# Optimization experiments

Measured on AMD Instinct MI355X. Metric: run time of the kernel, lower is better.

The kernel has to match this reference:

```python
import jax, jax.numpy as jnp
import numpy as np

B, S, H = 1, 2048, 3584
NH, NKV, D = 16, 8, 256
GROUPS = NH // NKV
WINDOW = 1024
SOFTCAP = 50.0
SCALING = 256.0 ** -0.5  # query_pre_attn_scalar ** -0.5
MASK_VAL = -1e9


def rotate_half(x):
    x1, x2 = jnp.split(x, 2, axis=-1)
    return jnp.concatenate([-x2, x1], axis=-1)


def setup_inputs() -> dict:
    key = jax.random.key(0)
    ks = jax.random.split(key, 5)
    hidden_states = jax.random.normal(ks[0], (B, S, H), dtype=jnp.float32)
    # real rotary embeddings, HF convention: [B, S, head_dim]
    inv_freq = 1.0 / (10000.0 ** (np.arange(0, D, 2, dtype=np.float32) / D))
    freqs = np.arange(S, dtype=np.float32)[:, None] * inv_freq[None, :]  # [S, D/2]
    emb = np.concatenate([freqs, freqs], axis=-1)  # [S, D]
    cos = jnp.asarray(np.cos(emb))[None]  # [1, S, D]
    sin = jnp.asarray(np.sin(emb))[None]
    sc = 1.0 / np.sqrt(H)
    wq = jax.random.normal(ks[1], (NH * D, H), dtype=jnp.float32) * sc
    wk = jax.random.normal(ks[2], (NKV * D, H), dtype=jnp.float32) * sc
    wv = jax.random.normal(ks[3], (NKV * D, H), dtype=jnp.float32) * sc
    wo = jax.random.normal(ks[4], (H, NH * D), dtype=jnp.float32) * (1.0 / np.sqrt(NH * D))
    return {"hidden_states": hidden_states, "cos": cos, "sin": sin,
            "wq": wq, "wk": wk, "wv": wv, "wo": wo}


def reference(hidden_states, cos, sin, wq, wk, wv, wo):
    # QKV projections -> [B, n_heads, S, D]
    q = jnp.einsum('bsh,oh->bso', hidden_states, wq).reshape(B, S, NH, D).transpose(0, 2, 1, 3)
    k = jnp.einsum('bsh,oh->bso', hidden_states, wk).reshape(B, S, NKV, D).transpose(0, 2, 1, 3)
    v = jnp.einsum('bsh,oh->bso', hidden_states, wv).reshape(B, S, NKV, D).transpose(0, 2, 1, 3)
    # RoPE (cos/sin broadcast over head dim)
    c = cos[:, None, :, :]
    s = sin[:, None, :, :]
    q = q * c + rotate_half(q) * s
    k = k * c + rotate_half(k) * s
    # GQA: repeat KV heads
    k = jnp.repeat(k, GROUPS, axis=1)  # [B, NH, S, D]
    v = jnp.repeat(v, GROUPS, axis=1)
    # scores + logit soft-capping (tanh), then causal + sliding-window mask
    scores = jnp.einsum('bhqd,bhkd->bhqk', q, k) * SCALING
    scores = SOFTCAP * jnp.tanh(scores / SOFTCAP)
    idx = jnp.arange(S)
    allowed = (idx[None, :] <= idx[:, None]) & (idx[:, None] - idx[None, :] < WINDOW)  # [S, S]
    scores = jnp.where(allowed[None, None], scores, MASK_VAL)
    p = jax.nn.softmax(scores, axis=-1)
    out = jnp.einsum('bhqk,bhkd->bhqd', p, v)  # [B, NH, S, D]
    out = out.transpose(0, 2, 1, 3).reshape(B, S, NH * D)
    return jnp.einsum('bso,ho->bsh', out, wo)
```

## Files before the change

### kernel.cpp

```cpp
#include <hip/hip_runtime.h>
#include <stdint.h>

#define S_LEN 2048
#define HDIM  3584
#define NHEAD 16
#define NKVH  8
#define DHEAD 256
#define QD    (NHEAD * DHEAD)
#define KD    (NKVH * DHEAD)
#define QKVD  (QD + 2 * KD)
#define WINDOW 1024
#define MASK_VAL (-1e9f)

typedef __bf16 bf16x8 __attribute__((ext_vector_type(8)));
typedef float  f32x4  __attribute__((ext_vector_type(4)));

__device__ __forceinline__ float bf2f(ushort u) {
    union { uint32_t i; float f; } v; v.i = ((uint32_t)u) << 16; return v.f;
}
__device__ __forceinline__ ushort f2bf(float f) {
    union { float f; uint32_t i; } v; v.f = f;
    uint32_t r = (v.i + 0x7FFF + ((v.i >> 16) & 1)) >> 16;
    return (ushort)r;
}
__device__ __forceinline__ void gll16(const ushort* g, ushort* l) {
    __builtin_amdgcn_global_load_lds(
        (const __attribute__((address_space(1))) void*)g,
        (__attribute__((address_space(3))) void*)l, 16, 0, 0);
}

__global__ __launch_bounds__(256) void cvt_kernel(const float* __restrict__ src,
                                                  ushort* __restrict__ dst, int n8)
{
    int i = blockIdx.x * blockDim.x + threadIdx.x;
    if (i >= n8) return;
    float4 a = ((const float4*)src)[i * 2];
    float4 b = ((const float4*)src)[i * 2 + 1];
    ushort tmp[8];
    tmp[0] = f2bf(a.x); tmp[1] = f2bf(a.y); tmp[2] = f2bf(a.z); tmp[3] = f2bf(a.w);
    tmp[4] = f2bf(b.x); tmp[5] = f2bf(b.y); tmp[6] = f2bf(b.z); tmp[7] = f2bf(b.w);
    ((uint4*)dst)[i] = *(uint4*)tmp;
}

__device__ __forceinline__ void stage_f32(ushort* __restrict__ dst,
                                          const float* __restrict__ src,
                                          int r0, int K, int kt, int t)
{
#pragma unroll
    for (int i = 0; i < 4; i++) {
        int g = t + i * 256;
        int row = g >> 3, c = g & 7;
        float4 f = *(const float4*)(src + (size_t)(r0 + row) * K + kt + c * 4);
        ushort4 u;
        u.x = f2bf(f.x); u.y = f2bf(f.y); u.z = f2bf(f.z); u.w = f2bf(f.w);
        *(ushort4*)(dst + row * 32 + c * 4) = u;
    }
}

template <typename TA, typename TC>
__global__ __launch_bounds__(256) void gemm_async(const TA* __restrict__ A,
                                                  const ushort* __restrict__ B,
                                                  TC* __restrict__ C,
                                                  int M, int N, int K)
{
    __shared__ __align__(16) ushort As[128 * 32];
    __shared__ __align__(16) ushort Bs[128 * 32];

    const int t    = threadIdx.x;
    const int lane = t & 63;
    const int w    = t >> 6;
    const int l15  = lane & 15;
    const int quad = lane >> 4;
    const int m0   = blockIdx.y * 128;
    const int n0   = blockIdx.x * 128;
    const int wm   = (w >> 1) * 64;
    const int wn   = (w & 1) * 64;
    const int srow = lane >> 2;
    const int scol = (lane & 3) * 8;

    f32x4 acc[4][4] = {};

    for (int kt = 0; kt < K; kt += 32) {
        __syncthreads();
#pragma unroll
        for (int j = 0; j < 2; j++) {
            const int rb = w * 32 + j * 16;
            if constexpr (sizeof(TA) == 2) {
                gll16((const ushort*)A + (size_t)(m0 + rb + srow) * K + kt + scol,
                      As + rb * 32);
            }
            gll16(B + (size_t)(n0 + rb + srow) * K + kt + scol, Bs + rb * 32);
        }
        if constexpr (sizeof(TA) == 4)
            stage_f32(As, (const float*)A, m0, K, kt, t);
        __syncthreads();

        bf16x8 a[4], b[4];
#pragma unroll
        for (int mi = 0; mi < 4; mi++)
            a[mi] = *(const bf16x8*)(As + (wm + mi * 16 + l15) * 32 + quad * 8);
#pragma unroll
        for (int ni = 0; ni < 4; ni++)
            b[ni] = *(const bf16x8*)(Bs + (wn + ni * 16 + l15) * 32 + quad * 8);
#pragma unroll
        for (int mi = 0; mi < 4; mi++)
#pragma unroll
            for (int ni = 0; ni < 4; ni++)
                acc[mi][ni] = __builtin_amdgcn_mfma_f32_16x16x32_bf16(
                    a[mi], b[ni], acc[mi][ni], 0, 0, 0);
    }

#pragma unroll
    for (int mi = 0; mi < 4; mi++)
#pragma unroll
        for (int ni = 0; ni < 4; ni++)
#pragma unroll
            for (int r = 0; r < 4; r++) {
                int row = m0 + wm + mi * 16 + quad * 4 + r;
                int col = n0 + wn + ni * 16 + l15;
                float val = acc[mi][ni][r];
                if constexpr (sizeof(TC) == 4) C[(size_t)row * N + col] = val;
                else                           C[(size_t)row * N + col] = f2bf(val);
            }
}

__global__ __launch_bounds__(256) void gemm_sync(const float* __restrict__ A,
                                                 const float* __restrict__ B,
                                                 ushort* __restrict__ C,
                                                 int M, int N, int K)
{
    __shared__ __align__(16) ushort As[128 * 32];
    __shared__ __align__(16) ushort Bs[128 * 32];
    const int t = threadIdx.x, lane = t & 63, w = t >> 6;
    const int l15 = lane & 15, quad = lane >> 4;
    const int m0 = blockIdx.y * 128, n0 = blockIdx.x * 128;
    const int wm = (w >> 1) * 64, wn = (w & 1) * 64;
    f32x4 acc[4][4] = {};
    for (int kt = 0; kt < K; kt += 32) {
        __syncthreads();
        stage_f32(As, A, m0, K, kt, t);
        stage_f32(Bs, B, n0, K, kt, t);
        __syncthreads();
        bf16x8 a[4], b[4];
#pragma unroll
        for (int mi = 0; mi < 4; mi++)
            a[mi] = *(const bf16x8*)(As + (wm + mi * 16 + l15) * 32 + quad * 8);
#pragma unroll
        for (int ni = 0; ni < 4; ni++)
            b[ni] = *(const bf16x8*)(Bs + (wn + ni * 16 + l15) * 32 + quad * 8);
#pragma unroll
        for (int mi = 0; mi < 4; mi++)
#pragma unroll
            for (int ni = 0; ni < 4; ni++)
                acc[mi][ni] = __builtin_amdgcn_mfma_f32_16x16x32_bf16(
                    a[mi], b[ni], acc[mi][ni], 0, 0, 0);
    }
#pragma unroll
    for (int mi = 0; mi < 4; mi++)
#pragma unroll
        for (int ni = 0; ni < 4; ni++)
#pragma unroll
            for (int r = 0; r < 4; r++)
                C[(size_t)(m0 + wm + mi * 16 + quad * 4 + r) * N +
                  n0 + wn + ni * 16 + l15] = f2bf(acc[mi][ni][r]);
}

__global__ __launch_bounds__(256) void gemm_sync_hf(const ushort* __restrict__ A,
                                                    const float* __restrict__ B,
                                                    float* __restrict__ C,
                                                    int M, int N, int K)
{
    __shared__ __align__(16) ushort As[128 * 32];
    __shared__ __align__(16) ushort Bs[128 * 32];
    const int t = threadIdx.x, lane = t & 63, w = t >> 6;
    const int l15 = lane & 15, quad = lane >> 4;
    const int m0 = blockIdx.y * 128, n0 = blockIdx.x * 128;
    const int wm = (w >> 1) * 64, wn = (w & 1) * 64;
    f32x4 acc[4][4] = {};
    for (int kt = 0; kt < K; kt += 32) {
        __syncthreads();
#pragma unroll
        for (int i = 0; i < 2; i++) {
            int g = t + i * 256;
            int row = g >> 2, c = g & 3;
            *(uint4*)(As + row * 32 + c * 8) =
                *(const uint4*)(A + (size_t)(m0 + row) * K + kt + c * 8);
        }
        stage_f32(Bs, B, n0, K, kt, t);
        __syncthreads();
        bf16x8 a[4], b[4];
#pragma unroll
        for (int mi = 0; mi < 4; mi++)
            a[mi] = *(const bf16x8*)(As + (wm + mi * 16 + l15) * 32 + quad * 8);
#pragma unroll
        for (int ni = 0; ni < 4; ni++)
            b[ni] = *(const bf16x8*)(Bs + (wn + ni * 16 + l15) * 32 + quad * 8);
#pragma unroll
        for (int mi = 0; mi < 4; mi++)
#pragma unroll
            for (int ni = 0; ni < 4; ni++)
                acc[mi][ni] = __builtin_amdgcn_mfma_f32_16x16x32_bf16(
                    a[mi], b[ni], acc[mi][ni], 0, 0, 0);
    }
#pragma unroll
    for (int mi = 0; mi < 4; mi++)
#pragma unroll
        for (int ni = 0; ni < 4; ni++)
#pragma unroll
            for (int r = 0; r < 4; r++)
                C[(size_t)(m0 + wm + mi * 16 + quad * 4 + r) * N +
                  n0 + wn + ni * 16 + l15] = acc[mi][ni][r];
}

__global__ void rope_kernel(ushort* __restrict__ x, int stride,
                            const float* __restrict__ cosb,
                            const float* __restrict__ sinb, int nh)
{
    int idx  = blockIdx.x * blockDim.x + threadIdx.x;
    int d    = idx & 127;
    int rest = idx >> 7;
    int h    = rest & (nh - 1);
    int s    = rest / nh;
    size_t base = (size_t)s * stride + h * DHEAD;
    float c  = cosb[s * DHEAD + d];
    float sn = sinb[s * DHEAD + d];
    float x1 = bf2f(x[base + d]);
    float x2 = bf2f(x[base + d + 128]);
    x[base + d]       = f2bf(x1 * c - x2 * sn);
    x[base + d + 128] = f2bf(x2 * c + x1 * sn);
}

__global__ __launch_bounds__(256) void vtrans_kernel(const ushort* __restrict__ v,
                                                     int stride,
                                                     ushort* __restrict__ vt)
{
    __shared__ __align__(16) ushort tile[64][72];
    int s0 = blockIdx.x * 64, c0 = blockIdx.y * 64;
    int t  = threadIdx.x;
#pragma unroll
    for (int i = 0; i < 2; i++) {
        int cI = t + i * 256;
        int row = cI >> 3, c8 = cI & 7;
        *(uint4*)&tile[row][c8 * 8] =
            *(const uint4*)(v + (size_t)(s0 + row) * stride + c0 + c8 * 8);
    }
    __syncthreads();
#pragma unroll
    for (int i = 0; i < 2; i++) {
        int cI = t + i * 256;
        int crow = cI >> 3, s8 = cI & 7;
        ushort tmp[8];
#pragma unroll
        for (int j = 0; j < 8; j++) tmp[j] = tile[s8 * 8 + j][crow];
        *(uint4*)(vt + (size_t)(c0 + crow) * S_LEN + s0 + s8 * 8) = *(uint4*)tmp;
    }
}

template <typename TO>
__global__ __launch_bounds__(256) void attn_kernel(const ushort* __restrict__ qr, int qstride,
                                                   const ushort* __restrict__ kr, int kstride,
                                                   const ushort* __restrict__ vt,
                                                   TO* __restrict__ out)
{
    __shared__ __align__(16) ushort Ks[64 * 256];
    __shared__ __align__(16) ushort Vs[256 * 64];
    __shared__ __align__(16) ushort Ps[4][16 * 68];

    const int t    = threadIdx.x;
    const int lane = t & 63;
    const int w    = t >> 6;
    const int l15  = lane & 15;
    const int quad = lane >> 4;
    const int q0B  = blockIdx.x * 64;
    const int q0   = q0B + w * 16;
    const int h    = blockIdx.y;
    const int kvh  = h >> 1;

    bf16x8 aQ[8];
    const ushort* qrow = qr + (size_t)(q0 + l15) * qstride + h * DHEAD;
#pragma unroll
    for (int kk = 0; kk < 8; kk++)
        aQ[kk] = *(const bf16x8*)(qrow + kk * 32 + quad * 8);

    f32x4 oacc[16] = {};
    float m_i[4], l_i[4];
#pragma unroll
    for (int r = 0; r < 4; r++) { m_i[r] = -1e30f; l_i[r] = 0.f; }

    int km = q0B - (WINDOW - 1);
    if (km < 0) km = 0;
    km &= ~63;

    for (int kb = km; kb < q0B + 64; kb += 64) {
        __syncthreads();
#pragma unroll
        for (int i = 0; i < 8; i++) {
            int base = i * 256 + w * 64;
            int idx  = base + lane;
            int row = idx >> 5, c = idx & 31;
            int cs = c ^ (row & 7);
            gll16(kr + (size_t)(kb + row) * kstride + kvh * DHEAD + cs * 8,
                  Ks + base * 8);
        }
#pragma unroll
        for (int i = 0; i < 8; i++) {
            int base = i * 256 + w * 64;
            int idx  = base + lane;
            int row = idx >> 3, c = idx & 7;
            int cs = c ^ (row & 7);
            gll16(vt + (size_t)(kvh * DHEAD + row) * S_LEN + kb + cs * 8,
                  Vs + base * 8);
        }
        __syncthreads();

        f32x4 sc[4] = {};
#pragma unroll
        for (int ni = 0; ni < 4; ni++) {
            int row = ni * 16 + l15;
#pragma unroll
            for (int kk = 0; kk < 8; kk++) {
                int cp = (kk * 4 + quad) ^ (row & 7);
                bf16x8 bk = *(const bf16x8*)(Ks + row * 256 + cp * 8);
                sc[ni] = __builtin_amdgcn_mfma_f32_16x16x32_bf16(aQ[kk], bk, sc[ni], 0, 0, 0);
            }
        }

        float p[4][4];
        float mt[4] = { -1e30f, -1e30f, -1e30f, -1e30f };
#pragma unroll
        for (int ni = 0; ni < 4; ni++)
#pragma unroll
            for (int r = 0; r < 4; r++) {
                int qi = q0 + quad * 4 + r;
                int ki = kb + ni * 16 + l15;
                float x = sc[ni][r] * 0.0625f;
                float e = __expf(x * 0.04f);
                x = 50.f * (e - 1.f) / (e + 1.f);
                bool ok = (ki <= qi) && (qi - ki < WINDOW);
                x = ok ? x : MASK_VAL;
                p[ni][r] = x;
                mt[r] = fmaxf(mt[r], x);
            }
#pragma unroll
        for (int r = 0; r < 4; r++)
#pragma unroll
            for (int off = 1; off < 16; off <<= 1)
                mt[r] = fmaxf(mt[r], __shfl_xor(mt[r], off));

        float alpha[4], rs[4];
#pragma unroll
        for (int r = 0; r < 4; r++) {
            float mn = fmaxf(m_i[r], mt[r]);
            alpha[r] = __expf(m_i[r] - mn);
            m_i[r] = mn;
            rs[r] = 0.f;
        }
#pragma unroll
        for (int ni = 0; ni < 4; ni++)
#pragma unroll
            for (int r = 0; r < 4; r++) {
                float pe = __expf(p[ni][r] - m_i[r]);
                rs[r] += pe;
                Ps[w][(quad * 4 + r) * 68 + ni * 16 + l15] = f2bf(pe);
            }
#pragma unroll
        for (int r = 0; r < 4; r++) {
#pragma unroll
            for (int off = 1; off < 16; off <<= 1)
                rs[r] += __shfl_xor(rs[r], off);
            l_i[r] = l_i[r] * alpha[r] + rs[r];
        }
#pragma unroll
        for (int nd = 0; nd < 16; nd++)
#pragma unroll
            for (int r = 0; r < 4; r++)
                oacc[nd][r] *= alpha[r];

        __asm__ volatile("s_waitcnt lgkmcnt(0)" ::: "memory");

        bf16x8 aP[2];
#pragma unroll
        for (int kk = 0; kk < 2; kk++)
            aP[kk] = *(const bf16x8*)(&Ps[w][l15 * 68 + kk * 32 + quad * 8]);
#pragma unroll
        for (int nd = 0; nd < 16; nd++) {
            int row = nd * 16 + l15;
#pragma unroll
            for (int kk = 0; kk < 2; kk++) {
                int cp = (kk * 4 + quad) ^ (row & 7);
                bf16x8 bv = *(const bf16x8*)(Vs + row * 64 + cp * 8);
                oacc[nd] = __builtin_amdgcn_mfma_f32_16x16x32_bf16(aP[kk], bv, oacc[nd], 0, 0, 0);
            }
        }
    }

#pragma unroll
    for (int nd = 0; nd < 16; nd++)
#pragma unroll
        for (int r = 0; r < 4; r++) {
            int qi = q0 + quad * 4 + r;
            int d  = nd * 16 + l15;
            float val = oacc[nd][r] / l_i[r];
            if constexpr (sizeof(TO) == 4) out[(size_t)qi * QD + h * DHEAD + d] = val;
            else                           out[(size_t)qi * QD + h * DHEAD + d] = f2bf(val);
        }
}

extern "C" void kernel_launch(void* const* d_in, const int* in_sizes, int n_in,
                              void* d_out, int out_size, void* d_ws, size_t ws_size,
                              hipStream_t stream)
{
    const float* hidden = (const float*)d_in[0];
    const float* cosb   = (const float*)d_in[1];
    const float* sinb   = (const float*)d_in[2];
    const float* wq     = (const float*)d_in[3];
    const float* wk     = (const float*)d_in[4];
    const float* wv     = (const float*)d_in[5];
    const float* wo     = (const float*)d_in[6];
    float* outp = (float*)d_out;

    const size_t nH   = (size_t)S_LEN * HDIM;
    const size_t nWQ  = (size_t)QD * HDIM;
    const size_t nWK  = (size_t)KD * HDIM;
    const size_t nWB  = (size_t)QKVD * HDIM;
    const size_t nQKV = (size_t)S_LEN * QKVD;
    const size_t nAT  = (size_t)S_LEN * QD;
    const size_t nVT  = (size_t)S_LEN * KD;

    dim3 blk(256);
    const size_t needA = (nH + nWB + nQKV) * 2;
    const size_t needB = (nWB + nQKV) * 2;

    if (ws_size >= needB) {
        const bool haveHb = ws_size >= needA;
        ushort* wb  = (ushort*)d_ws;
        ushort* qkv = wb + nWB;
        ushort* hb  = qkv + nQKV;
        ushort* at  = wb;
        ushort* vtb = wb + nAT;
        ushort* ob  = wb + nAT + nVT;

        cvt_kernel<<<(int)(nWQ / 8 / 256), blk, 0, stream>>>(wq, wb, (int)(nWQ / 8));
        cvt_kernel<<<(int)(nWK / 8 / 256), blk, 0, stream>>>(wk, wb + nWQ, (int)(nWK / 8));
        cvt_kernel<<<(int)(nWK / 8 / 256), blk, 0, stream>>>(wv, wb + nWQ + nWK, (int)(nWK / 8));

        if (haveHb) {
            cvt_kernel<<<(int)(nH / 8 / 256), blk, 0, stream>>>(hidden, hb, (int)(nH / 8));
            gemm_async<ushort, ushort><<<dim3(QKVD / 128, S_LEN / 128), blk, 0, stream>>>(
                hb, wb, qkv, S_LEN, QKVD, HDIM);
        } else {
            gemm_async<float, ushort><<<dim3(QKVD / 128, S_LEN / 128), blk, 0, stream>>>(
                hidden, wb, qkv, S_LEN, QKVD, HDIM);
        }

        cvt_kernel<<<(int)(nWQ / 8 / 256), blk, 0, stream>>>(wo, ob, (int)(nWQ / 8));

        rope_kernel<<<(S_LEN * NHEAD * 128) / 256, blk, 0, stream>>>(qkv, QKVD, cosb, sinb, NHEAD);
        rope_kernel<<<(S_LEN * NKVH * 128) / 256, blk, 0, stream>>>(qkv + QD, QKVD, cosb, sinb, NKVH);
        vtrans_kernel<<<dim3(S_LEN / 64, KD / 64), blk, 0, stream>>>(qkv + QD + KD, QKVD, vtb);

        attn_kernel<ushort><<<dim3(S_LEN / 64, NHEAD), blk, 0, stream>>>(
            qkv, QKVD, qkv + QD, QKVD, vtb, at);

        gemm_async<ushort, float><<<dim3(HDIM / 128, S_LEN / 128), blk, 0, stream>>>(
            at, ob, outp, S_LEN, HDIM, QD);
    } else {
        ushort* q  = (ushort*)d_ws;
        ushort* k  = q + nAT;
        ushort* v  = k + nVT;
        ushort* vtb = v + nVT;
        ushort* at = vtb + nVT;

        gemm_sync<<<dim3(QD / 128, S_LEN / 128), blk, 0, stream>>>(hidden, wq, q, S_LEN, QD, HDIM);
        gemm_sync<<<dim3(KD / 128, S_LEN / 128), blk, 0, stream>>>(hidden, wk, k, S_LEN, KD, HDIM);
        gemm_sync<<<dim3(KD / 128, S_LEN / 128), blk, 0, stream>>>(hidden, wv, v, S_LEN, KD, HDIM);
        rope_kernel<<<(S_LEN * NHEAD * 128) / 256, blk, 0, stream>>>(q, QD, cosb, sinb, NHEAD);
        rope_kernel<<<(S_LEN * NKVH * 128) / 256, blk, 0, stream>>>(k, KD, cosb, sinb, NKVH);
        vtrans_kernel<<<dim3(S_LEN / 64, KD / 64), blk, 0, stream>>>(v, KD, vtb);
        attn_kernel<ushort><<<dim3(S_LEN / 64, NHEAD), blk, 0, stream>>>(q, QD, k, KD, vtb, at);
        gemm_sync_hf<<<dim3(HDIM / 128, S_LEN / 128), blk, 0, stream>>>(at, wo, outp, S_LEN, HDIM, QD);
    }
}
```

Measured before the change: 652.2 us.

## Swizzle GEMM LDS tiles, fuse conversions, and skip masking on interior attention blocks

Applies an XOR swizzle to the LDS tile layout in all three GEMM variants, so the 16-byte fragment reads by the MFMA lanes spread across banks instead of conflicting. Merges the five fp32-to-bf16 conversion launches into one kernel that needs a larger workspace. In attention, interior key blocks skip the causal and window mask check, and the tanh divide and final normalisation divide become reciprocal multiplies. The risks are the bigger workspace requirement, which falls back to the older path if not met, and the slightly less exact rcp approximation.

```diff
diff --git a/kernel.cpp b/kernel.cpp
--- a/kernel.cpp
+++ b/kernel.cpp
@@ -29,6 +29,33 @@
         (__attribute__((address_space(3))) void*)l, 16, 0, 0);
 }
 
+#define N_H8  (S_LEN * HDIM / 8)
+#define N_WQ8 (QD * HDIM / 8)
+#define N_WK8 (KD * HDIM / 8)
+#define N_WO8 (HDIM * QD / 8)
+#define N_CVT (N_H8 + N_WQ8 + 2 * N_WK8 + N_WO8)
+
+__global__ __launch_bounds__(256) void cvt5_kernel(
+    const float* __restrict__ hid, const float* __restrict__ wq,
+    const float* __restrict__ wk,  const float* __restrict__ wv,
+    const float* __restrict__ wo,
+    ushort* __restrict__ hb, ushort* __restrict__ wb, ushort* __restrict__ ob)
+{
+    int j = blockIdx.x * blockDim.x + threadIdx.x;
+    const float* s; ushort* d;
+    if (j < N_H8)                { s = hid; d = hb; }
+    else if ((j -= N_H8) < N_WQ8)  { s = wq; d = wb; }
+    else if ((j -= N_WQ8) < N_WK8) { s = wk; d = wb + (size_t)QD * HDIM; }
+    else if ((j -= N_WK8) < N_WK8) { s = wv; d = wb + (size_t)(QD + KD) * HDIM; }
+    else                         { j -= N_WK8; s = wo; d = ob; }
+    float4 a = ((const float4*)s)[(size_t)j * 2];
+    float4 b = ((const float4*)s)[(size_t)j * 2 + 1];
+    ushort tmp[8];
+    tmp[0] = f2bf(a.x); tmp[1] = f2bf(a.y); tmp[2] = f2bf(a.z); tmp[3] = f2bf(a.w);
+    tmp[4] = f2bf(b.x); tmp[5] = f2bf(b.y); tmp[6] = f2bf(b.z); tmp[7] = f2bf(b.w);
+    ((uint4*)d)[j] = *(uint4*)tmp;
+}
+
 __global__ __launch_bounds__(256) void cvt_kernel(const float* __restrict__ src,
                                                   ushort* __restrict__ dst, int n8)
 {
@@ -53,7 +80,8 @@
         float4 f = *(const float4*)(src + (size_t)(r0 + row) * K + kt + c * 4);
         ushort4 u;
         u.x = f2bf(f.x); u.y = f2bf(f.y); u.z = f2bf(f.z); u.w = f2bf(f.w);
-        *(ushort4*)(dst + row * 32 + c * 4) = u;
+        int cl = (c >> 1) ^ ((row >> 1) & 3);
+        *(ushort4*)(dst + row * 32 + cl * 8 + (c & 1) * 4) = u;
     }
 }
 
@@ -76,7 +104,8 @@
     const int wm   = (w >> 1) * 64;
     const int wn   = (w & 1) * 64;
     const int srow = lane >> 2;
-    const int scol = (lane & 3) * 8;
+    const int scol = ((lane & 3) ^ ((srow >> 1) & 3)) * 8;
+    const int sw   = (l15 >> 1) & 3;
 
     f32x4 acc[4][4] = {};
 
@@ -98,10 +127,10 @@
         bf16x8 a[4], b[4];
 #pragma unroll
         for (int mi = 0; mi < 4; mi++)
-            a[mi] = *(const bf16x8*)(As + (wm + mi * 16 + l15) * 32 + quad * 8);
-#pragma unroll
-        for (int ni = 0; ni < 4; ni++)
-            b[ni] = *(const bf16x8*)(Bs + (wn + ni * 16 + l15) * 32 + quad * 8);
+            a[mi] = *(const bf16x8*)(As + (wm + mi * 16 + l15) * 32 + (quad ^ sw) * 8);
+#pragma unroll
+        for (int ni = 0; ni < 4; ni++)
+            b[ni] = *(const bf16x8*)(Bs + (wn + ni * 16 + l15) * 32 + (quad ^ sw) * 8);
 #pragma unroll
         for (int mi = 0; mi < 4; mi++)
 #pragma unroll
@@ -133,6 +162,7 @@
     __shared__ __align__(16) ushort Bs[128 * 32];
     const int t = threadIdx.x, lane = t & 63, w = t >> 6;
     const int l15 = lane & 15, quad = lane >> 4;
+    const int sw = (l15 >> 1) & 3;
     const int m0 = blockIdx.y * 128, n0 = blockIdx.x * 128;
     const int wm = (w >> 1) * 64, wn = (w & 1) * 64;
     f32x4 acc[4][4] = {};
@@ -144,10 +174,10 @@
         bf16x8 a[4], b[4];
 #pragma unroll
         for (int mi = 0; mi < 4; mi++)
-            a[mi] = *(const bf16x8*)(As + (wm + mi * 16 + l15) * 32 + quad * 8);
-#pragma unroll
-        for (int ni = 0; ni < 4; ni++)
-            b[ni] = *(const bf16x8*)(Bs + (wn + ni * 16 + l15) * 32 + quad * 8);
+            a[mi] = *(const bf16x8*)(As + (wm + mi * 16 + l15) * 32 + (quad ^ sw) * 8);
+#pragma unroll
+        for (int ni = 0; ni < 4; ni++)
+            b[ni] = *(const bf16x8*)(Bs + (wn + ni * 16 + l15) * 32 + (quad ^ sw) * 8);
 #pragma unroll
         for (int mi = 0; mi < 4; mi++)
 #pragma unroll
@@ -174,6 +204,7 @@
     __shared__ __align__(16) ushort Bs[128 * 32];
     const int t = threadIdx.x, lane = t & 63, w = t >> 6;
     const int l15 = lane & 15, quad = lane >> 4;
+    const int sw = (l15 >> 1) & 3;
     const int m0 = blockIdx.y * 128, n0 = blockIdx.x * 128;
     const int wm = (w >> 1) * 64, wn = (w & 1) * 64;
     f32x4 acc[4][4] = {};
@@ -183,7 +214,8 @@
         for (int i = 0; i < 2; i++) {
             int g = t + i * 256;
             int row = g >> 2, c = g & 3;
-            *(uint4*)(As + row * 32 + c * 8) =
+            int cl = c ^ ((row >> 1) & 3);
+            *(uint4*)(As + row * 32 + cl * 8) =
                 *(const uint4*)(A + (size_t)(m0 + row) * K + kt + c * 8);
         }
         stage_f32(Bs, B, n0, K, kt, t);
@@ -191,10 +223,10 @@
         bf16x8 a[4], b[4];
 #pragma unroll
         for (int mi = 0; mi < 4; mi++)
-            a[mi] = *(const bf16x8*)(As + (wm + mi * 16 + l15) * 32 + quad * 8);
-#pragma unroll
-        for (int ni = 0; ni < 4; ni++)
-            b[ni] = *(const bf16x8*)(Bs + (wn + ni * 16 + l15) * 32 + quad * 8);
+            a[mi] = *(const bf16x8*)(As + (wm + mi * 16 + l15) * 32 + (quad ^ sw) * 8);
+#pragma unroll
+        for (int ni = 0; ni < 4; ni++)
+            b[ni] = *(const bf16x8*)(Bs + (wn + ni * 16 + l15) * 32 + (quad ^ sw) * 8);
 #pragma unroll
         for (int mi = 0; mi < 4; mi++)
 #pragma unroll
@@ -325,22 +357,34 @@
             }
         }
 
+        const bool interior = (kb + 63 <= q0) && (q0 + 15 - kb < WINDOW);
         float p[4][4];
         float mt[4] = { -1e30f, -1e30f, -1e30f, -1e30f };
-#pragma unroll
-        for (int ni = 0; ni < 4; ni++)
-#pragma unroll
-            for (int r = 0; r < 4; r++) {
-                int qi = q0 + quad * 4 + r;
-                int ki = kb + ni * 16 + l15;
-                float x = sc[ni][r] * 0.0625f;
-                float e = __expf(x * 0.04f);
-                x = 50.f * (e - 1.f) / (e + 1.f);
-                bool ok = (ki <= qi) && (qi - ki < WINDOW);
-                x = ok ? x : MASK_VAL;
-                p[ni][r] = x;
-                mt[r] = fmaxf(mt[r], x);
-            }
+        if (interior) {
+#pragma unroll
+            for (int ni = 0; ni < 4; ni++)
+#pragma unroll
+                for (int r = 0; r < 4; r++) {
+                    float e = __expf(sc[ni][r] * 0.0025f);
+                    float x = 50.f * (e - 1.f) * __builtin_amdgcn_rcpf(e + 1.f);
+                    p[ni][r] = x;
+                    mt[r] = fmaxf(mt[r], x);
+                }
+        } else {
+#pragma unroll
+            for (int ni = 0; ni < 4; ni++)
+#pragma unroll
+                for (int r = 0; r < 4; r++) {
+                    int qi = q0 + quad * 4 + r;
+                    int ki = kb + ni * 16 + l15;
+                    float e = __expf(sc[ni][r] * 0.0025f);
+                    float x = 50.f * (e - 1.f) * __builtin_amdgcn_rcpf(e + 1.f);
+                    bool ok = (ki <= qi) && (qi - ki < WINDOW);
+                    x = ok ? x : MASK_VAL;
+                    p[ni][r] = x;
+                    mt[r] = fmaxf(mt[r], x);
+                }
+        }
 #pragma unroll
         for (int r = 0; r < 4; r++)
 #pragma unroll
@@ -395,15 +439,17 @@
     }
 
 #pragma unroll
-    for (int nd = 0; nd < 16; nd++)
-#pragma unroll
-        for (int r = 0; r < 4; r++) {
+    for (int r = 0; r < 4; r++) {
+        float invl = __builtin_amdgcn_rcpf(l_i[r]);
+#pragma unroll
+        for (int nd = 0; nd < 16; nd++) {
             int qi = q0 + quad * 4 + r;
             int d  = nd * 16 + l15;
-            float val = oacc[nd][r] / l_i[r];
+            float val = oacc[nd][r] * invl;
             if constexpr (sizeof(TO) == 4) out[(size_t)qi * QD + h * DHEAD + d] = val;
             else                           out[(size_t)qi * QD + h * DHEAD + d] = f2bf(val);
         }
+    }
 }
 
 extern "C" void kernel_launch(void* const* d_in, const int* in_sizes, int n_in,
@@ -423,19 +469,36 @@
     const size_t nWQ  = (size_t)QD * HDIM;
     const size_t nWK  = (size_t)KD * HDIM;
     const size_t nWB  = (size_t)QKVD * HDIM;
+    const size_t nWO  = (size_t)HDIM * QD;
     const size_t nQKV = (size_t)S_LEN * QKVD;
     const size_t nAT  = (size_t)S_LEN * QD;
     const size_t nVT  = (size_t)S_LEN * KD;
 
     dim3 blk(256);
-    const size_t needA = (nH + nWB + nQKV) * 2;
+    const size_t needA = (nWB + nQKV + nH + nWO) * 2;
     const size_t needB = (nWB + nQKV) * 2;
 
-    if (ws_size >= needB) {
-        const bool haveHb = ws_size >= needA;
+    if (ws_size >= needA) {
         ushort* wb  = (ushort*)d_ws;
         ushort* qkv = wb + nWB;
         ushort* hb  = qkv + nQKV;
+        ushort* ob  = hb + nH;
+        ushort* at  = wb;
+        ushort* vtb = wb + nAT;
+
+        cvt5_kernel<<<(N_CVT + 255) / 256, blk, 0, stream>>>(hidden, wq, wk, wv, wo, hb, wb, ob);
+        gemm_async<ushort, ushort><<<dim3(QKVD / 128, S_LEN / 128), blk, 0, stream>>>(
+            hb, wb, qkv, S_LEN, QKVD, HDIM);
+        rope_kernel<<<(S_LEN * NHEAD * 128) / 256, blk, 0, stream>>>(qkv, QKVD, cosb, sinb, NHEAD);
+        rope_kernel<<<(S_LEN * NKVH * 128) / 256, blk, 0, stream>>>(qkv + QD, QKVD, cosb, sinb, NKVH);
+        vtrans_kernel<<<dim3(S_LEN / 64, KD / 64), blk, 0, stream>>>(qkv + QD + KD, QKVD, vtb);
+        attn_kernel<ushort><<<dim3(S_LEN / 64, NHEAD), blk, 0, stream>>>(
+            qkv, QKVD, qkv + QD, QKVD, vtb, at);
+        gemm_async<ushort, float><<<dim3(HDIM / 128, S_LEN / 128), blk, 0, stream>>>(
+            at, ob, outp, S_LEN, HDIM, QD);
+    } else if (ws_size >= needB) {
+        ushort* wb  = (ushort*)d_ws;
+        ushort* qkv = wb + nWB;
         ushort* at  = wb;
         ushort* vtb = wb + nAT;
         ushort* ob  = wb + nAT + nVT;
@@ -443,33 +506,22 @@
         cvt_kernel<<<(int)(nWQ / 8 / 256), blk, 0, stream>>>(wq, wb, (int)(nWQ / 8));
         cvt_kernel<<<(int)(nWK / 8 / 256), blk, 0, stream>>>(wk, wb + nWQ, (int)(nWK / 8));
         cvt_kernel<<<(int)(nWK / 8 / 256), blk, 0, stream>>>(wv, wb + nWQ + nWK, (int)(nWK / 8));
-
-        if (haveHb) {
-            cvt_kernel<<<(int)(nH / 8 / 256), blk, 0, stream>>>(hidden, hb, (int)(nH / 8));
-            gemm_async<ushort, ushort><<<dim3(QKVD / 128, S_LEN / 128), blk, 0, stream>>>(
-                hb, wb, qkv, S_LEN, QKVD, HDIM);
-        } else {
-            gemm_async<float, ushort><<<dim3(QKVD / 128, S_LEN / 128), blk, 0, stream>>>(
-                hidden, wb, qkv, S_LEN, QKVD, HDIM);
-        }
-
-        cvt_kernel<<<(int)(nWQ / 8 / 256), blk, 0, stream>>>(wo, ob, (int)(nWQ / 8));
-
+        gemm_async<float, ushort><<<dim3(QKVD / 128, S_LEN / 128), blk, 0, stream>>>(
+            hidden, wb, qkv, S_LEN, QKVD, HDIM);
+        cvt_kernel<<<(int)(nWO / 8 / 256), blk, 0, stream>>>(wo, ob, (int)(nWO / 8));
         rope_kernel<<<(S_LEN * NHEAD * 128) / 256, blk, 0, stream>>>(qkv, QKVD, cosb, sinb, NHEAD);
         rope_kernel<<<(S_LEN * NKVH * 128) / 256, blk, 0, stream>>>(qkv + QD, QKVD, cosb, sinb, NKVH);
         vtrans_kernel<<<dim3(S_LEN / 64, KD / 64), blk, 0, stream>>>(qkv + QD + KD, QKVD, vtb);
-
         attn_kernel<ushort><<<dim3(S_LEN / 64, NHEAD), blk, 0, stream>>>(
             qkv, QKVD, qkv + QD, QKVD, vtb, at);
-
         gemm_async<ushort, float><<<dim3(HDIM / 128, S_LEN / 128), blk, 0, stream>>>(
             at, ob, outp, S_LEN, HDIM, QD);
     } else {
-        ushort* q  = (ushort*)d_ws;
-        ushort* k  = q + nAT;
-        ushort* v  = k + nVT;
+        ushort* q   = (ushort*)d_ws;
+        ushort* k   = q + nAT;
+        ushort* v   = k + nVT;
         ushort* vtb = v + nVT;
-        ushort* at = vtb + nVT;
+        ushort* at  = vtb + nVT;
 
         gemm_sync<<<dim3(QD / 128, S_LEN / 128), blk, 0, stream>>>(hidden, wq, q, S_LEN, QD, HDIM);
         gemm_sync<<<dim3(KD / 128, S_LEN / 128), blk, 0, stream>>>(hidden, wk, k, S_LEN, KD, HDIM);
```

New measurement: 622.6 us. 4.5% less time.
